# Kernel optimization log

Measured on AMD Instinct MI355X. Metric: run time of the kernel, lower is better.

The kernel has to match this reference:

```python
import jax, jax.numpy as jnp
import numpy as np

DIM = 384
HEADS = 12
WS = 7
HID = 4 * 256  # FFN hidden is hard-coded default 1024, NOT 4*dim
EPS = 1e-5


def layernorm(x, g, b):
    mu = jnp.mean(x, axis=-1, keepdims=True)
    var = jnp.mean(jnp.square(x - mu), axis=-1, keepdims=True)
    return (x - mu) * jax.lax.rsqrt(var + EPS) * g + b


def setup_inputs() -> dict:
    key = jax.random.key(0)
    ks = jax.random.split(key, 12)
    s = 0.02
    return {
        "x": jax.random.normal(ks[0], (32, DIM, 56, 56), dtype=jnp.float32),
        "ln1_g": jnp.ones((DIM,), jnp.float32),
        "ln1_b": jnp.zeros((DIM,), jnp.float32),
        "qkv_w": jax.random.normal(ks[1], (3 * DIM, DIM), jnp.float32) * s,
        "qkv_b": jnp.zeros((3 * DIM,), jnp.float32),
        "proj_w": jax.random.normal(ks[2], (DIM, DIM), jnp.float32) * s,
        "proj_b": jnp.zeros((DIM,), jnp.float32),
        "ln2_g": jnp.ones((DIM,), jnp.float32),
        "ln2_b": jnp.zeros((DIM,), jnp.float32),
        "fc1_w": jax.random.normal(ks[3], (HID, DIM), jnp.float32) * s,
        "fc1_b": jnp.zeros((HID,), jnp.float32),
        "fc2_w": jax.random.normal(ks[4], (DIM, HID), jnp.float32) * s,
        "fc2_b": jnp.zeros((DIM,), jnp.float32),
    }


def window_attention(x, qkv_w, qkv_b, proj_w, proj_b):
    # x: [B, H, W, C] channels-last
    B, H, W, C = x.shape
    Wh, Ww = H // WS, W // WS
    # partition: [B*Wh*Ww, WS*WS, C]
    w = x.reshape(B, Wh, WS, Ww, WS, C).transpose(0, 1, 3, 2, 4, 5)
    w = w.reshape(B * Wh * Ww, WS * WS, C)
    Bn, N, _ = w.shape
    hd = C // HEADS
    qkv = w @ qkv_w.T + qkv_b  # [Bn, N, 3C]
    qkv = qkv.reshape(Bn, N, 3, HEADS, hd).transpose(2, 0, 3, 1, 4)
    q, k, v = qkv[0], qkv[1], qkv[2]  # each [Bn, h, N, hd]
    attn = jnp.einsum('bhnd,bhmd->bhnm', q, k) * (hd ** -0.5)
    attn = jax.nn.softmax(attn, axis=-1)
    o = jnp.einsum('bhnm,bhmd->bhnd', attn, v)
    o = o.transpose(0, 2, 1, 3).reshape(Bn, N, C)
    o = o @ proj_w.T + proj_b
    # reverse
    o = o.reshape(B, Wh, Ww, WS, WS, C).transpose(0, 1, 3, 2, 4, 5)
    return o.reshape(B, H, W, C)


def reference(x, ln1_g, ln1_b, qkv_w, qkv_b, proj_w, proj_b,
              ln2_g, ln2_b, fc1_w, fc1_b, fc2_w, fc2_b):
    # x: [B, C, H, W]
    residual = x
    h = x.transpose(0, 2, 3, 1)  # [B,H,W,C]
    h = layernorm(h, ln1_g, ln1_b)
    h = window_attention(h, qkv_w, qkv_b, proj_w, proj_b)
    x = h.transpose(0, 3, 1, 2) + residual
    residual = x
    h = x.transpose(0, 2, 3, 1)
    h = layernorm(h, ln2_g, ln2_b)
    h = jax.nn.gelu(h @ fc1_w.T + fc1_b, approximate=False)
    h = h @ fc2_w.T + fc2_b
    return h.transpose(0, 3, 1, 2) + residual
```

## Files before the change

kernel.cpp:

```cpp
#include <hip/hip_runtime.h>
#include <cstdint>
#include <cmath>

#define DIM 384
#define HEADS 12
#define TOKENS 100352
#define HW_ 3136
#define NWIN 2048

typedef __attribute__((ext_vector_type(8))) short short8;
typedef __attribute__((ext_vector_type(4))) short short4v;
typedef __attribute__((ext_vector_type(2))) short short2v;
typedef __attribute__((ext_vector_type(4))) float f32x4;

#define AS1 __attribute__((address_space(1)))
#define AS3 __attribute__((address_space(3)))

__device__ __forceinline__ short f2b(float f){
  unsigned u = __builtin_bit_cast(unsigned, f);
  u += 0x7FFFu + ((u >> 16) & 1u);
  return (short)(u >> 16);
}
__device__ __forceinline__ float b2f(short h){
  unsigned u = ((unsigned)(unsigned short)h) << 16;
  return __builtin_bit_cast(float, u);
}

__device__ __forceinline__ void gload_lds16(const short* g, short* l){
  __builtin_amdgcn_global_load_lds((AS1 void*)(g), (AS3 void*)(l), 16, 0, 0);
}

__device__ __forceinline__ float gelu_f(float v){
  float z  = v * 0.70710678118654752f;
  float az = fabsf(z);
  float t  = __builtin_amdgcn_rcpf(1.f + 0.3275911f*az);
  float poly = t*(0.254829592f + t*(-0.284496736f + t*(1.421413741f +
               t*(-1.453152027f + t*1.061405429f))));
  float e  = __expf(-z*z);
  float er = copysignf(1.f - poly*e, z);
  return 0.5f * v * (1.f + er);
}

__global__ __launch_bounds__(256) void k_cvt4(
    const float* __restrict__ s0, const float* __restrict__ s1,
    const float* __restrict__ s2, const float* __restrict__ s3,
    short* __restrict__ d0, short* __restrict__ d1,
    short* __restrict__ d2, short* __restrict__ d3)
{
  int i = blockIdx.x*256 + threadIdx.x;
  if (i < 442368) d0[i] = f2b(s0[i]);
  if (i < 147456) d1[i] = f2b(s1[i]);
  if (i < 393216){ d2[i] = f2b(s2[i]); d3[i] = f2b(s3[i]); }
}

__global__ __launch_bounds__(256) void k_ln1(const float* __restrict__ x,
    const float* __restrict__ gam, const float* __restrict__ bet,
    short* __restrict__ ln1, short* __restrict__ xr)
{
  __shared__ float red0[256];
  __shared__ float red1[256];
  __shared__ float mus[64], rss[64];
  __shared__ short xfull[64*388];
  int t = threadIdx.x;
  int blk = blockIdx.x;
  int b = blk / 49;
  int hw0 = (blk % 49) * 64;
  int p = t & 63, cq = t >> 6;
  const float* xb = x + (long)b*DIM*HW_ + hw0 + p;
  float s = 0.f, sq = 0.f;
  for (int i = 0; i < 96; i++){
    int c = i*4 + cq;
    float v = xb[(long)c*HW_];
    s += v; sq += v*v;
    xfull[p*388 + c] = f2b(v);
  }
  red0[t] = s; red1[t] = sq;
  __syncthreads();
  if (t < 64){
    float ts = red0[t] + red0[t+64] + red0[t+128] + red0[t+192];
    float tq = red1[t] + red1[t+64] + red1[t+128] + red1[t+192];
    float mu = ts * (1.f/DIM);
    float var = tq * (1.f/DIM) - mu*mu;
    mus[t] = mu;
    rss[t] = rsqrtf(var + 1e-5f);
  }
  __syncthreads();
  int p2 = t >> 2, q4 = t & 3;
  float mu = mus[p2], rs = rss[p2];
  int hwp2 = hw0 + p2;
  int h2 = hwp2 / 56, w2 = hwp2 % 56;
  int wt2 = ((b*8 + h2/7)*8 + w2/7)*49 + (h2%7)*7 + (w2%7);
  long lnbase = (long)wt2*DIM;
  long xrbase = (long)(b*HW_ + hwp2)*DIM;
  #pragma unroll
  for (int cc0 = 0; cc0 < DIM; cc0 += 32){
    short8 xv = *(const short8*)(xfull + p2*388 + cc0 + q4*8);
    short8 lv;
    #pragma unroll
    for (int u = 0; u < 8; u++){
      int c = cc0 + q4*8 + u;
      float v = b2f(xv[u]);
      lv[u] = f2b((v - mu)*rs*gam[c] + bet[c]);
    }
    *(short8*)(ln1 + lnbase + cc0 + q4*8) = lv;
    *(short8*)(xr + xrbase + cc0 + q4*8) = xv;
  }
}

#define EPI_BIAS 0
#define EPI_PROJ 1
#define EPI_GELU 2
#define EPI_OUT  4

template<int EPI>
__global__ __launch_bounds__(256) void k_gemm(
    const short* __restrict__ A, const short* __restrict__ B,
    const float* __restrict__ bias, short* __restrict__ out,
    const short* __restrict__ res, int M, int N, int K, int ntiles)
{
  constexpr int ES = (EPI == EPI_OUT) ? 133 : 132;
  __shared__ short sm[20480];
  float* E = (float*)sm;

  int nwg = gridDim.x;
  int orig = blockIdx.x;
  int bid = (orig & 7) * (nwg >> 3) + (orig >> 3);
  int nt = bid % ntiles, mt = bid / ntiles;
  int m0 = mt*128, n0 = nt*128;
  int t = threadIdx.x;
  int lane = t & 63, wv = t >> 6;
  int wm = wv >> 1, wn = wv & 1;
  int gg = lane >> 4, cc = lane & 15;

  int srow = t >> 2;
  int skc = ((t & 3) ^ (srow & 3)) << 3;
  const short* Ab = A + (long)(m0 + srow)*K + skc;
  const short* Bb = B + (long)(n0 + srow)*K + skc;
  long rowstep = 64L*K;

  int goff = (gg << 3) ^ ((cc & 3) << 3);

  f32x4 acc[4][4];
  #pragma unroll
  for (int i=0;i<4;i++)
    #pragma unroll
    for (int j=0;j<4;j++) acc[i][j] = (f32x4){0.f,0.f,0.f,0.f};

  int nk = K >> 5;

  gload_lds16(Ab,           sm + t*8);
  gload_lds16(Ab + rowstep, sm + (t+256)*8);
  gload_lds16(Bb,           sm + 12288 + t*8);
  gload_lds16(Bb + rowstep, sm + 12288 + (t+256)*8);
  gload_lds16(Ab + 32,           sm + 4096 + t*8);
  gload_lds16(Ab + 32 + rowstep, sm + 4096 + (t+256)*8);

  int ac = 0, bc = 0;
  for (int kt = 0; kt < nk; kt++){
    if (kt + 1 < nk) { asm volatile("s_waitcnt vmcnt(2) lgkmcnt(0)" ::: "memory"); }
    else             { asm volatile("s_waitcnt vmcnt(0) lgkmcnt(0)" ::: "memory"); }
    __builtin_amdgcn_s_barrier();
    if (kt + 1 < nk){
      long ko = (long)(kt+1) << 5;
      int bn = bc ^ 1;
      gload_lds16(Bb + ko,           sm + 12288 + bn*4096 + t*8);
      gload_lds16(Bb + ko + rowstep, sm + 12288 + bn*4096 + (t+256)*8);
    }
    if (kt + 2 < nk){
      long ko = (long)(kt+2) << 5;
      int an = ac + 2; if (an >= 3) an -= 3;
      gload_lds16(Ab + ko,           sm + an*4096 + t*8);
      gload_lds16(Ab + ko + rowstep, sm + an*4096 + (t+256)*8);
    }
    const short* Ac = sm + ac*4096;
    const short* Bc = sm + 12288 + bc*4096;
    short8 af[4], bfv[4];
    #pragma unroll
    for (int mi=0;mi<4;mi++) af[mi] = *(const short8*)(Ac + (wm*64 + mi*16 + cc)*32 + goff);
    #pragma unroll
    for (int ni=0;ni<4;ni++) bfv[ni] = *(const short8*)(Bc + (wn*64 + ni*16 + cc)*32 + goff);
    #pragma unroll
    for (int mi=0;mi<4;mi++)
      #pragma unroll
      for (int ni=0;ni<4;ni++)
        acc[mi][ni] = __builtin_amdgcn_mfma_f32_16x16x32_bf16(af[mi], bfv[ni], acc[mi][ni], 0, 0, 0);
    ac = (ac + 1 == 3) ? 0 : ac + 1;
    bc ^= 1;
  }

  if constexpr (EPI == EPI_OUT) {
    float* outf = (float*)out;
    #pragma unroll
    for (int p = 0; p < 2; p++){
      __syncthreads();
      if (wm == p){
        #pragma unroll
        for (int mi=0;mi<4;mi++){
          #pragma unroll
          for (int r=0;r<4;r++){
            float* Er = E + (mi*16 + gg*4 + r)*ES + wn*64 + cc;
            Er[0]  = acc[mi][0][r];
            Er[16] = acc[mi][1][r];
            Er[32] = acc[mi][2][r];
            Er[48] = acc[mi][3][r];
          }
        }
      }
      __syncthreads();
      #pragma unroll
      for (int jj = 0; jj < 8; jj++){
        int unit = jj*256 + t;
        int crow = unit >> 5, chunk = unit & 31;
        int row = m0 + p*64 + crow;
        f32x4 v = *(const f32x4*)(E + crow*ES + chunk*4);
        f32x4 bv = *(const f32x4*)(bias + n0 + chunk*4);
        short4v rv = *(const short4v*)(res + (long)row*N + n0 + chunk*4);
        #pragma unroll
        for (int j = 0; j < 4; j++) v[j] += bv[j] + b2f(rv[j]);
        *(f32x4*)(E + crow*ES + chunk*4) = v;
      }
      __syncthreads();
      #pragma unroll
      for (int jj = 0; jj < 32; jj++){
        int unit = jj*256 + t;
        int c = unit >> 6, rl = unit & 63;
        int token = m0 + p*64 + rl;
        int b = token / HW_;
        int hw = token - b*HW_;
        outf[((long)b*DIM + n0 + c)*HW_ + hw] = E[rl*ES + c];
      }
    }
  } else {
    #pragma unroll
    for (int p = 0; p < 2; p++){
      __syncthreads();
      #pragma unroll
      for (int mh = 0; mh < 2; mh++){
        #pragma unroll
        for (int r = 0; r < 4; r++){
          int crow = wm*32 + mh*16 + gg*4 + r;
          float* Er = E + crow*ES + wn*64 + cc;
          Er[0]  = acc[mh*2 + p][0][r];
          Er[16] = acc[mh*2 + p][1][r];
          Er[32] = acc[mh*2 + p][2][r];
          Er[48] = acc[mh*2 + p][3][r];
        }
      }
      __syncthreads();
      #pragma unroll
      for (int jj = 0; jj < 8; jj++){
        int unit = jj*256 + t;
        int crow = unit >> 5, chunk = unit & 31;
        int rr = crow & 15, mh = (crow >> 4) & 1, wmr = crow >> 5;
        int row = m0 + wmr*64 + (mh*2 + p)*16 + rr;
        int col = n0 + chunk*4;
        f32x4 v = *(const f32x4*)(E + crow*ES + chunk*4);
        f32x4 bv = *(const f32x4*)(bias + col);
        long orow;
        if constexpr (EPI == EPI_PROJ) {
          int b = row / HW_; int rem = row % HW_;
          int wid = rem / 49, idx = rem % 49;
          int hh = (wid >> 3)*7 + idx/7;
          int ww = (wid & 7)*7 + idx%7;
          orow = (long)(b*HW_ + hh*56 + ww)*N;
        } else {
          orow = (long)row*N;
        }
        float vv[4];
        #pragma unroll
        for (int j = 0; j < 4; j++){
          vv[j] = v[j] + bv[j];
          if constexpr (EPI == EPI_GELU) vv[j] = gelu_f(vv[j]);
        }
        if constexpr (EPI == EPI_PROJ){
          short4v rv = *(const short4v*)(res + orow + col);
          #pragma unroll
          for (int j = 0; j < 4; j++) vv[j] += b2f(rv[j]);
        }
        short4v ov;
        #pragma unroll
        for (int j = 0; j < 4; j++) ov[j] = f2b(vv[j]);
        *(short4v*)(out + orow + col) = ov;
      }
    }
  }
}

__global__ __launch_bounds__(256) void k_ln2(const short* __restrict__ x2,
  const float* __restrict__ gam, const float* __restrict__ bet, short* __restrict__ o)
{
  int t = threadIdx.x, lane = t & 63, wv = t >> 6;
  long row = (long)blockIdx.x*4 + wv;
  const short* xr = x2 + row*DIM;
  short4v a = *(const short4v*)(xr + lane*4);
  short2v b2 = *(const short2v*)(xr + 256 + lane*2);
  float f[6] = {b2f(a[0]),b2f(a[1]),b2f(a[2]),b2f(a[3]),b2f(b2[0]),b2f(b2[1])};
  float s = 0.f, sq = 0.f;
  #pragma unroll
  for (int i=0;i<6;i++){ s += f[i]; sq += f[i]*f[i]; }
  #pragma unroll
  for (int off=1; off<64; off<<=1){ s += __shfl_xor(s, off); sq += __shfl_xor(sq, off); }
  float mu = s*(1.f/DIM);
  float var = sq*(1.f/DIM) - mu*mu;
  float rs = rsqrtf(var + 1e-5f);
  int c0 = lane*4, c1 = 256 + lane*2;
  short4v oa; short2v ob;
  #pragma unroll
  for (int i=0;i<4;i++) oa[i] = f2b((f[i]-mu)*rs*gam[c0+i] + bet[c0+i]);
  #pragma unroll
  for (int j=0;j<2;j++) ob[j] = f2b((f[4+j]-mu)*rs*gam[c1+j] + bet[c1+j]);
  *(short4v*)(o + row*DIM + c0) = oa;
  *(short2v*)(o + row*DIM + c1) = ob;
}

__global__ __launch_bounds__(256) void k_attn(const short* __restrict__ qkv, short* __restrict__ o)
{
  __shared__ short lds[4*7424];
  int t = threadIdx.x;
  int lane = t & 63, wv = t >> 6;
  int w = blockIdx.x;
  int h = wv + (int)blockIdx.y*4;
  short* Qs = lds + wv*7424;
  short* Ks = Qs + 2560;
  short* Vt = Ks + 2560;
  short* Pl = Qs;
  int g = lane >> 4, c = lane & 15;
  int nrow = lane >> 2;
  int dc = (lane & 3) * 8;
  const float scale = 0.17677669529663687f;

  long base = (long)w*49*1152 + h*32;
  #pragma unroll
  for (int it = 0; it < 4; it++){
    int n = it*16 + nrow;
    short8 vq = {0,0,0,0,0,0,0,0};
    short8 vk = vq, vvv = vq;
    if (n < 49){
      vq  = *(const short8*)(qkv + base + (long)n*1152 + dc);
      vk  = *(const short8*)(qkv + base + (long)n*1152 + 384 + dc);
      vvv = *(const short8*)(qkv + base + (long)n*1152 + 768 + dc);
    }
    *(short8*)(Qs + n*40 + dc) = vq;
    *(short8*)(Ks + n*40 + dc) = vk;
    #pragma unroll
    for (int u = 0; u < 8; u++) Vt[(dc+u)*72 + n] = vvv[u];
  }
  asm volatile("s_waitcnt lgkmcnt(0)" ::: "memory");
  __builtin_amdgcn_sched_barrier(0);

  f32x4 sacc[4][4];
  #pragma unroll
  for (int i=0;i<4;i++)
    #pragma unroll
    for (int j=0;j<4;j++) sacc[i][j] = (f32x4){0.f,0.f,0.f,0.f};
  short8 kf[4];
  #pragma unroll
  for (int ni=0;ni<4;ni++) kf[ni] = *(const short8*)(Ks + (ni*16 + c)*40 + g*8);
  #pragma unroll
  for (int mi=0;mi<4;mi++){
    short8 a = *(const short8*)(Qs + (mi*16 + c)*40 + g*8);
    #pragma unroll
    for (int ni=0;ni<4;ni++)
      sacc[mi][ni] = __builtin_amdgcn_mfma_f32_16x16x32_bf16(a, kf[ni], sacc[mi][ni], 0, 0, 0);
  }
  #pragma unroll
  for (int mi=0;mi<4;mi++){
    #pragma unroll
    for (int r=0;r<4;r++){
      float v0 = sacc[mi][0][r]*scale;
      float v1 = sacc[mi][1][r]*scale;
      float v2 = sacc[mi][2][r]*scale;
      float v3 = (c >= 1) ? -1e30f : sacc[mi][3][r]*scale;
      float mx = fmaxf(fmaxf(v0,v1), fmaxf(v2,v3));
      #pragma unroll
      for (int off=1; off<16; off<<=1) mx = fmaxf(mx, __shfl_xor(mx, off));
      float e0 = __expf(v0-mx), e1 = __expf(v1-mx), e2 = __expf(v2-mx), e3 = __expf(v3-mx);
      float sm = e0+e1+e2+e3;
      #pragma unroll
      for (int off=1; off<16; off<<=1) sm += __shfl_xor(sm, off);
      float inv = 1.f/sm;
      int prow = mi*16 + g*4 + r;
      Pl[prow*72 +      c] = f2b(e0*inv);
      Pl[prow*72 + 16 + c] = f2b(e1*inv);
      Pl[prow*72 + 32 + c] = f2b(e2*inv);
      Pl[prow*72 + 48 + c] = f2b(e3*inv);
    }
  }
  asm volatile("s_waitcnt lgkmcnt(0)" ::: "memory");
  __builtin_amdgcn_sched_barrier(0);

  f32x4 oacc[4][2];
  #pragma unroll
  for (int i=0;i<4;i++){ oacc[i][0] = (f32x4){0.f,0.f,0.f,0.f}; oacc[i][1] = oacc[i][0]; }
  #pragma unroll
  for (int ks=0; ks<2; ks++){
    short8 bb0 = *(const short8*)(Vt + (c)*72      + ks*32 + g*8);
    short8 bb1 = *(const short8*)(Vt + (16 + c)*72 + ks*32 + g*8);
    #pragma unroll
    for (int mi=0;mi<4;mi++){
      short8 aa = *(const short8*)(Pl + (mi*16 + c)*72 + ks*32 + g*8);
      oacc[mi][0] = __builtin_amdgcn_mfma_f32_16x16x32_bf16(aa, bb0, oacc[mi][0], 0, 0, 0);
      oacc[mi][1] = __builtin_amdgcn_mfma_f32_16x16x32_bf16(aa, bb1, oacc[mi][1], 0, 0, 0);
    }
  }
  #pragma unroll
  for (int mi=0;mi<4;mi++){
    #pragma unroll
    for (int r=0;r<4;r++){
      int row = mi*16 + g*4 + r;
      if (row < 49){
        long ob = ((long)w*49 + row)*384 + h*32;
        o[ob + c]      = f2b(oacc[mi][0][r]);
        o[ob + 16 + c] = f2b(oacc[mi][1][r]);
      }
    }
  }
}

extern "C" void kernel_launch(void* const* d_in, const int* in_sizes, int n_in,
                              void* d_out, int out_size, void* d_ws, size_t ws_size,
                              hipStream_t stream) {
  (void)in_sizes; (void)n_in; (void)out_size; (void)ws_size;
  const float* x      = (const float*)d_in[0];
  const float* ln1_g  = (const float*)d_in[1];
  const float* ln1_b  = (const float*)d_in[2];
  const float* qkv_w  = (const float*)d_in[3];
  const float* qkv_b  = (const float*)d_in[4];
  const float* proj_w = (const float*)d_in[5];
  const float* proj_b = (const float*)d_in[6];
  const float* ln2_g  = (const float*)d_in[7];
  const float* ln2_b  = (const float*)d_in[8];
  const float* fc1_w  = (const float*)d_in[9];
  const float* fc1_b  = (const float*)d_in[10];
  const float* fc2_w  = (const float*)d_in[11];
  const float* fc2_b  = (const float*)d_in[12];

  char* ws = (char*)d_ws;
  short* buf1 = (short*)(ws);
  short* buf2 = (short*)(ws + 231211008L);
  short* buf3 = (short*)(ws + 308281344L);
  short* buf4 = (short*)(ws + 385351680L);
  short* buf5 = (short*)(ws + 462422016L);
  short* wq = (short*)(ws + 539492352L);
  short* wp = wq + 442368;
  short* w1 = wp + 147456;
  short* w2 = w1 + 393216;

  k_cvt4<<<dim3(1728), dim3(256), 0, stream>>>(qkv_w, proj_w, fc1_w, fc2_w,
                                               wq, wp, w1, w2);

  k_ln1<<<dim3(1568), dim3(256), 0, stream>>>(x, ln1_g, ln1_b, buf2, buf5);

  k_gemm<EPI_BIAS><<<dim3(784*9), dim3(256), 0, stream>>>(buf2, wq, qkv_b, buf1, nullptr,
                                                          TOKENS, 1152, 384, 9);
  k_attn<<<dim3(NWIN, 3), dim3(256), 0, stream>>>(buf1, buf3);

  k_gemm<EPI_PROJ><<<dim3(784*3), dim3(256), 0, stream>>>(buf3, wp, proj_b, buf4, buf5,
                                                          TOKENS, 384, 384, 3);
  k_ln2<<<dim3(TOKENS/4), dim3(256), 0, stream>>>(buf4, ln2_g, ln2_b, buf2);

  k_gemm<EPI_GELU><<<dim3(784*8), dim3(256), 0, stream>>>(buf2, w1, fc1_b, buf1, nullptr,
                                                          TOKENS, 1024, 384, 8);
  k_gemm<EPI_OUT><<<dim3(784*3), dim3(256), 0, stream>>>(buf1, w2, fc2_b, (short*)d_out, buf4,
                                                         TOKENS, 384, 1024, 3);
}
```

Measured before the change: 717.2 us.

## Add K=384 GEMM keeping whole B tile in LDS with 512-row M tiles

Adds a new GEMM kernel for the K=384 QKV and FC1 projections. It loads the entire 128x384 weight tile into LDS once, streams A fragments straight from global memory into registers with double buffering, and covers 512 rows per workgroup using 8 waves. It also swaps the workgroup swizzle for a bijective mapping that tolerates grid sizes not divisible by 8. The aim is to cut repeated B loads and K-loop LDS synchronisation. In exchange it uses a large LDS footprint, high register pressure from 32 accumulators, and a serialised per-wave epilogue.

```diff
diff --git a/kernel.cpp b/kernel.cpp
--- a/kernel.cpp
+++ b/kernel.cpp
@@ -28,6 +28,12 @@
 
 __device__ __forceinline__ void gload_lds16(const short* g, short* l){
   __builtin_amdgcn_global_load_lds((AS1 void*)(g), (AS3 void*)(l), 16, 0, 0);
+}
+
+__device__ __forceinline__ int bij_swz(int orig, int nwg){
+  int q = nwg >> 3, r = nwg & 7;
+  int x = orig & 7, w = orig >> 3;
+  return (x < r ? x*(q+1) : r*(q+1) + (x-r)*q) + w;
 }
 
 __device__ __forceinline__ float gelu_f(float v){
@@ -111,6 +117,99 @@
 #define EPI_PROJ 1
 #define EPI_GELU 2
 #define EPI_OUT  4
+
+template<int EPI>
+__global__ __launch_bounds__(512) void k_gemmB(
+    const short* __restrict__ A, const short* __restrict__ B,
+    const float* __restrict__ bias, short* __restrict__ out,
+    int M, int N, int ntiles)
+{
+  constexpr int K = 384;
+  constexpr int NK = 12;
+  __shared__ short smB[128*408];
+  float* E = (float*)smB;
+
+  int nwg = gridDim.x;
+  int bid = bij_swz(blockIdx.x, nwg);
+  int nt = bid % ntiles, mt = bid / ntiles;
+  int m0 = mt*512, n0 = nt*128;
+  int t = threadIdx.x;
+  int lane = t & 63, wv = t >> 6;
+  int gg = lane >> 4, cc = lane & 15;
+
+  #pragma unroll
+  for (int i = 0; i < 13; i++){
+    int u = t + i*512;
+    if (i < 12 || t < 384){
+      int row = u / 51, s = u - row*51;
+      gload_lds16(B + (long)(n0 + row)*K + s*8, smB + u*8);
+    }
+  }
+  asm volatile("s_waitcnt vmcnt(0)" ::: "memory");
+  __syncthreads();
+
+  const short* Ap = A + (long)(m0 + wv*64 + cc)*K + gg*8;
+  const long mstep = 16L*K;
+
+  f32x4 acc[4][8];
+  #pragma unroll
+  for (int i=0;i<4;i++)
+    #pragma unroll
+    for (int j=0;j<8;j++) acc[i][j] = (f32x4){0.f,0.f,0.f,0.f};
+
+  short8 a[2][4];
+  #pragma unroll
+  for (int mi=0;mi<4;mi++) a[0][mi] = *(const short8*)(Ap + mi*mstep);
+  #pragma unroll
+  for (int mi=0;mi<4;mi++) a[1][mi] = *(const short8*)(Ap + 32 + mi*mstep);
+
+  #pragma unroll
+  for (int kt = 0; kt < NK; kt++){
+    short8 bfr[8];
+    #pragma unroll
+    for (int ni=0;ni<8;ni++)
+      bfr[ni] = *(const short8*)(smB + (ni*16 + cc)*408 + kt*32 + gg*8);
+    #pragma unroll
+    for (int mi=0;mi<4;mi++)
+      #pragma unroll
+      for (int ni=0;ni<8;ni++)
+        acc[mi][ni] = __builtin_amdgcn_mfma_f32_16x16x32_bf16(a[kt&1][mi], bfr[ni], acc[mi][ni], 0, 0, 0);
+    if (kt + 2 < NK){
+      #pragma unroll
+      for (int mi=0;mi<4;mi++) a[kt&1][mi] = *(const short8*)(Ap + (kt+2)*32 + mi*mstep);
+    }
+  }
+
+  __syncthreads();
+  for (int pw = 0; pw < 8; pw++){
+    if (wv == pw){
+      #pragma unroll
+      for (int mi=0;mi<4;mi++)
+        #pragma unroll
+        for (int ni=0;ni<8;ni++)
+          #pragma unroll
+          for (int r=0;r<4;r++)
+            E[(mi*16 + gg*4 + r)*132 + ni*16 + cc] = acc[mi][ni][r];
+    }
+    __syncthreads();
+    #pragma unroll
+    for (int jj = 0; jj < 4; jj++){
+      int unit = jj*512 + t;
+      int crow = unit >> 5, chunk = unit & 31;
+      f32x4 v = *(const f32x4*)(E + crow*132 + chunk*4);
+      f32x4 bv = *(const f32x4*)(bias + n0 + chunk*4);
+      short4v ov;
+      #pragma unroll
+      for (int j = 0; j < 4; j++){
+        float vv = v[j] + bv[j];
+        if constexpr (EPI == EPI_GELU) vv = gelu_f(vv);
+        ov[j] = f2b(vv);
+      }
+      *(short4v*)(out + (long)(m0 + pw*64 + crow)*N + n0 + chunk*4) = ov;
+    }
+    __syncthreads();
+  }
+}
 
 template<int EPI>
 __global__ __launch_bounds__(256) void k_gemm(
@@ -451,16 +550,16 @@
 
   k_ln1<<<dim3(1568), dim3(256), 0, stream>>>(x, ln1_g, ln1_b, buf2, buf5);
 
-  k_gemm<EPI_BIAS><<<dim3(784*9), dim3(256), 0, stream>>>(buf2, wq, qkv_b, buf1, nullptr,
-                                                          TOKENS, 1152, 384, 9);
+  k_gemmB<EPI_BIAS><<<dim3(196*9), dim3(512), 0, stream>>>(buf2, wq, qkv_b, buf1,
+                                                           TOKENS, 1152, 9);
   k_attn<<<dim3(NWIN, 3), dim3(256), 0, stream>>>(buf1, buf3);
 
   k_gemm<EPI_PROJ><<<dim3(784*3), dim3(256), 0, stream>>>(buf3, wp, proj_b, buf4, buf5,
                                                           TOKENS, 384, 384, 3);
   k_ln2<<<dim3(TOKENS/4), dim3(256), 0, stream>>>(buf4, ln2_g, ln2_b, buf2);
 
-  k_gemm<EPI_GELU><<<dim3(784*8), dim3(256), 0, stream>>>(buf2, w1, fc1_b, buf1, nullptr,
-                                                          TOKENS, 1024, 384, 8);
+  k_gemmB<EPI_GELU><<<dim3(196*8), dim3(512), 0, stream>>>(buf2, w1, fc1_b, buf1,
+                                                           TOKENS, 1024, 8);
   k_gemm<EPI_OUT><<<dim3(784*3), dim3(256), 0, stream>>>(buf1, w2, fc2_b, (short*)d_out, buf4,
                                                          TOKENS, 384, 1024, 3);
 }
```

Result: slower. 818.0 us (+14.1%).
